# Kernel optimization log

Measured on AMD Instinct MI355X. Metric: run time of the kernel, lower is better.

The kernel has to match this reference:

```python
import jax, jax.numpy as jnp
import numpy as np

B, T, I, H = 4, 512, 128, 128


def _lstm(x, Wih, Whh, b):
    """Standard LSTM (PyTorch gate order i,f,g,o). x: [B,T,I] -> h: [B,T,H]."""
    xg = jnp.swapaxes(x, 0, 1) @ Wih.T + b  # [T,B,4H] input projections precomputed
    Hh = Whh.shape[1]
    h0 = jnp.zeros((x.shape[0], Hh), x.dtype)
    c0 = jnp.zeros((x.shape[0], Hh), x.dtype)

    def step(carry, xg_t):
        h, c = carry
        g = xg_t + h @ Whh.T
        i, f, gg, o = jnp.split(g, 4, axis=-1)
        c = jax.nn.sigmoid(f) * c + jax.nn.sigmoid(i) * jnp.tanh(gg)
        h = jax.nn.sigmoid(o) * jnp.tanh(c)
        return (h, c), h

    _, hs = jax.lax.scan(step, (h0, c0), xg)
    return jnp.swapaxes(hs, 0, 1)  # [B,T,H]


def setup_inputs() -> dict:
    key = jax.random.key(0)
    ks = jax.random.split(key, 12)
    s = 0.1
    return {
        "x": jax.random.normal(ks[0], (B, T, I), jnp.float32),
        # shared LSTM
        "Wih_s": jax.random.normal(ks[1], (4 * H, I), jnp.float32) * s,
        "Whh_s": jax.random.normal(ks[2], (4 * H, H), jnp.float32) * s,
        "b_lstm_s": jnp.zeros((4 * H,), jnp.float32),
        # Ws split along its concatenated input [x_sub; h_t; h_sub]
        "Wx": jax.random.normal(ks[3], (I, H), jnp.float32) * s,
        "Wht": jax.random.normal(ks[4], (H, H), jnp.float32) * s,
        "Whs": jax.random.normal(ks[5], (H, H), jnp.float32) * s,
        "bs": jnp.zeros((H,), jnp.float32),
        # Us: H -> 1
        "u": jax.random.normal(ks[6], (H,), jnp.float32) * s,
        "bu": jnp.zeros((), jnp.float32),
        # task LSTM over [x; R] (input_size + hidden_size)
        "Wih_t": jax.random.normal(ks[7], (4 * H, I + H), jnp.float32) * s,
        "Whh_t": jax.random.normal(ks[8], (4 * H, H), jnp.float32) * s,
        "b_lstm_t": jnp.zeros((4 * H,), jnp.float32),
    }


def reference(x, Wih_s, Whh_s, b_lstm_s, Wx, Wht, Whs, bs, u, bu,
              Wih_t, Whh_t, b_lstm_t):
    # 1) shared LSTM encoding
    Hsh = _lstm(x, Wih_s, Whh_s, b_lstm_s)  # [B,T,H]

    # 2) pairwise attention scores S[b,t,s] = Us(tanh(Ws([x_s; h_t; h_s])))
    #    decompose Ws over its concatenated input to avoid building the concat
    xp = x @ Wx          # [B,T,H] (indexed by s)
    hp_t = Hsh @ Wht     # [B,T,H] (indexed by t)
    hp_s = Hsh @ Whs     # [B,T,H] (indexed by s)
    # M[b,t,s,:]: [B,T,T,H] — the dominant (memory-bound) intermediate
    M = jnp.tanh(hp_t[:, :, None, :] + (xp + hp_s)[:, None, :, :] + bs)
    scores = jnp.einsum("btsh,h->bts", M, u) + bu  # [B,T,T]

    # 3) softmax over sub_t and weighted sum of shared outputs
    beta = jax.nn.softmax(scores, axis=-1)         # [B,T,T]
    R = jnp.einsum("bts,bsh->bth", beta, Hsh)      # [B,T,H]

    # 4) task-specific LSTM consuming the input and the aggregated message
    h_task = _lstm(jnp.concatenate([x, R], axis=-1), Wih_t, Whh_t, b_lstm_t)
    return h_task  # [B,T,H]
```

## Files before the change

### kernel.cpp

```cpp
#include <hip/hip_runtime.h>
#include <hip/hip_bf16.h>
#include <math.h>

#define Bq 4
#define Tq 512
#define Hq 128

typedef _Float16 f16x4 __attribute__((ext_vector_type(4)));
typedef _Float16 f16x8 __attribute__((ext_vector_type(8)));
typedef float f32x4 __attribute__((ext_vector_type(4)));

__device__ __forceinline__ float rcp_fast(float x) { return __builtin_amdgcn_rcpf(x); }
__device__ __forceinline__ float sigmoid_fast(float x) {
    return rcp_fast(1.0f + __expf(-x));
}
__device__ __forceinline__ float tanh_fast(float x) {
    float e = __expf(2.0f * x);
    return 1.0f - 2.0f * rcp_fast(e + 1.0f);
}

__device__ __forceinline__ void gemm_nt_body(float (*As)[68], float (*Ws)[68],
                                             const float* __restrict__ A, int lda,
                                             const float* __restrict__ W, int ldw,
                                             const float* __restrict__ bias,
                                             float* __restrict__ C, int acc_flag,
                                             int m0, int n0, int tid) {
    int tx = tid & 15, ty = tid >> 4;
    float acc[4][4] = {};
    for (int kc = 0; kc < 2; kc++) {
        __syncthreads();
#pragma unroll
        for (int i = 0; i < 4; i++) {
            int idx = tid + 256 * i;
            int r = idx >> 4, c4 = idx & 15;
            *(float4*)(&As[r][c4 * 4]) = *(const float4*)(A + (size_t)(m0 + r) * lda + kc * 64 + c4 * 4);
            *(float4*)(&Ws[r][c4 * 4]) = *(const float4*)(W + (size_t)(n0 + r) * ldw + kc * 64 + c4 * 4);
        }
        __syncthreads();
#pragma unroll
        for (int k4 = 0; k4 < 16; k4++) {
            float4 a[4], wv[4];
#pragma unroll
            for (int i = 0; i < 4; i++) a[i] = *(const float4*)(&As[ty * 4 + i][k4 * 4]);
#pragma unroll
            for (int j = 0; j < 4; j++) wv[j] = *(const float4*)(&Ws[tx * 4 + j][k4 * 4]);
#pragma unroll
            for (int i = 0; i < 4; i++)
#pragma unroll
                for (int j = 0; j < 4; j++)
                    acc[i][j] += a[i].x * wv[j].x + a[i].y * wv[j].y + a[i].z * wv[j].z + a[i].w * wv[j].w;
        }
    }
#pragma unroll
    for (int i = 0; i < 4; i++) {
        int m = m0 + ty * 4 + i;
        int n = n0 + tx * 4;
        float4 v = make_float4(acc[i][0], acc[i][1], acc[i][2], acc[i][3]);
        if (bias) { v.x += bias[n]; v.y += bias[n + 1]; v.z += bias[n + 2]; v.w += bias[n + 3]; }
        if (acc_flag) {
            float4 o = *(const float4*)(C + (size_t)m * 512 + n);
            v.x += o.x; v.y += o.y; v.z += o.z; v.w += o.w;
        }
        *(float4*)(C + (size_t)m * 512 + n) = v;
    }
}

__device__ __forceinline__ void gemm_nt_512(float (*As)[68], float (*Ws)[68],
                                            const float* __restrict__ A, int lda,
                                            const float* __restrict__ W, int ldw,
                                            const float* __restrict__ bias,
                                            float* __restrict__ C,
                                            int m0, int n0, int tid) {
    int tx = tid & 15, ty = tid >> 4;
    float acc[2][4] = {};
    for (int kc = 0; kc < 2; kc++) {
        __syncthreads();
#pragma unroll
        for (int i = 0; i < 2; i++) {
            int idx = tid + 512 * i;
            int r = idx >> 4, c4 = idx & 15;
            *(float4*)(&As[r][c4 * 4]) = *(const float4*)(A + (size_t)(m0 + r) * lda + kc * 64 + c4 * 4);
            *(float4*)(&Ws[r][c4 * 4]) = *(const float4*)(W + (size_t)(n0 + r) * ldw + kc * 64 + c4 * 4);
        }
        __syncthreads();
#pragma unroll
        for (int k4 = 0; k4 < 16; k4++) {
            float4 a[2], wv[4];
#pragma unroll
            for (int i = 0; i < 2; i++) a[i] = *(const float4*)(&As[ty * 2 + i][k4 * 4]);
#pragma unroll
            for (int j = 0; j < 4; j++) wv[j] = *(const float4*)(&Ws[tx * 4 + j][k4 * 4]);
#pragma unroll
            for (int i = 0; i < 2; i++)
#pragma unroll
                for (int j = 0; j < 4; j++)
                    acc[i][j] += a[i].x * wv[j].x + a[i].y * wv[j].y + a[i].z * wv[j].z + a[i].w * wv[j].w;
        }
    }
#pragma unroll
    for (int i = 0; i < 2; i++) {
        int m = m0 + ty * 2 + i;
        int n = n0 + tx * 4;
        float4 v = make_float4(acc[i][0], acc[i][1], acc[i][2], acc[i][3]);
        if (bias) { v.x += bias[n]; v.y += bias[n + 1]; v.z += bias[n + 2]; v.w += bias[n + 3]; }
        *(float4*)(C + (size_t)m * 512 + n) = v;
    }
}

__global__ __launch_bounds__(256) void prep(const float* __restrict__ x,
                                            const float* __restrict__ Wih_s,
                                            const float* __restrict__ b_s,
                                            const float* __restrict__ Whh_s,
                                            float* __restrict__ xg_s,
                                            _Float16* __restrict__ W16_s) {
    __shared__ __align__(16) float As[64][68];
    __shared__ __align__(16) float Ws[64][68];
    int bid = blockIdx.x;
    int tid = threadIdx.x;
    if (bid < 256) {
        gemm_nt_body(As, Ws, x, 128, Wih_s, 128, b_s, xg_s, 0,
                     (bid & 31) * 64, (bid >> 5) * 64, tid);
    } else {
        int cb = bid - 256;
        int i = (cb * 256 + tid) * 4;
        float4 v = *(const float4*)(Whh_s + i);
        f16x4 o;
        o[0] = (_Float16)v.x; o[1] = (_Float16)v.y;
        o[2] = (_Float16)v.z; o[3] = (_Float16)v.w;
        *(f16x4*)(W16_s + i) = o;
    }
}

__global__ __launch_bounds__(256) void gemm_nt(const float* __restrict__ A, int lda,
                                               const float* __restrict__ W, int ldw,
                                               const float* __restrict__ bias,
                                               float* __restrict__ C, int acc_flag) {
    __shared__ __align__(16) float As[64][68];
    __shared__ __align__(16) float Ws[64][68];
    gemm_nt_body(As, Ws, A, lda, W, ldw, bias, C, acc_flag,
                 blockIdx.x * 64, blockIdx.y * 64, threadIdx.x);
}

__global__ __launch_bounds__(256) void mid(const float* __restrict__ x,
                                           const float* __restrict__ Hsh,
                                           const float* __restrict__ Wht,
                                           const float* __restrict__ Wx,
                                           const float* __restrict__ Whs,
                                           const float* __restrict__ bs,
                                           float* __restrict__ hp_t,
                                           float* __restrict__ tc_sT) {
    __shared__ __align__(16) float As[64][68];
    __shared__ __align__(16) float Bs[64][68];
    int bid = blockIdx.x;
    int cfg = bid >> 6;
    int b2 = bid & 63;
    int m0 = (b2 & 31) * 64, n0 = (b2 >> 5) * 64;
    const float* A1 = cfg ? x : Hsh;
    const float* B1 = cfg ? Wx : Wht;
    const float* A2 = cfg ? Hsh : nullptr;
    const float* B2 = cfg ? Whs : nullptr;

    int tid = threadIdx.x;
    int tx = tid & 15, ty = tid >> 4;
    float acc[4][4] = {};
    for (int src = 0; src < 2; src++) {
        const float* A = src ? A2 : A1;
        const float* Bm = src ? B2 : B1;
        if (!A) break;
        for (int kc = 0; kc < 2; kc++) {
            __syncthreads();
#pragma unroll
            for (int i = 0; i < 4; i++) {
                int idx = tid + 256 * i;
                int r = idx >> 4, c4 = idx & 15;
                *(float4*)(&As[r][c4 * 4]) = *(const float4*)(A + (size_t)(m0 + r) * 128 + kc * 64 + c4 * 4);
                *(float4*)(&Bs[r][c4 * 4]) = *(const float4*)(Bm + (size_t)(kc * 64 + r) * 128 + n0 + c4 * 4);
            }
            __syncthreads();
#pragma unroll
            for (int k4 = 0; k4 < 16; k4++) {
                float4 a[4];
#pragma unroll
                for (int i = 0; i < 4; i++) a[i] = *(const float4*)(&As[ty * 4 + i][k4 * 4]);
#pragma unroll
                for (int kk = 0; kk < 4; kk++) {
                    float4 bv = *(const float4*)(&Bs[k4 * 4 + kk][tx * 4]);
#pragma unroll
                    for (int i = 0; i < 4; i++) {
                        float av = (kk == 0) ? a[i].x : (kk == 1) ? a[i].y : (kk == 2) ? a[i].z : a[i].w;
                        acc[i][0] += av * bv.x;
                        acc[i][1] += av * bv.y;
                        acc[i][2] += av * bv.z;
                        acc[i][3] += av * bv.w;
                    }
                }
            }
        }
    }
    if (cfg == 0) {
#pragma unroll
        for (int i = 0; i < 4; i++) {
            int m = m0 + ty * 4 + i;
            int n = n0 + tx * 4;
            *(float4*)(hp_t + (size_t)m * 128 + n) =
                make_float4(acc[i][0], acc[i][1], acc[i][2], acc[i][3]);
        }
    } else {
        __syncthreads();
#pragma unroll
        for (int i = 0; i < 4; i++)
#pragma unroll
            for (int j = 0; j < 4; j++)
                As[ty * 4 + i][tx * 4 + j] = tanh_fast(acc[i][j] + bs[n0 + tx * 4 + j]);
        __syncthreads();
        int b = m0 >> 9;
        int s0 = m0 & 511;
        int lane = tid & 63, wv = tid >> 6;
#pragma unroll 4
        for (int it = 0; it < 16; ++it) {
            int nl = wv * 16 + it;
            tc_sT[((size_t)(b * 128 + n0 + nl)) * 512 + s0 + lane] = As[lane][nl];
        }
    }
}

#define MF0(ACC, A, B) \
    asm("v_mfma_f32_16x16x32_f16 %0, %1, %2, %3" : "=&v"(ACC) : "v"(A), "a"(B), "v"(zro));
#define MF(ACC, A, B) \
    asm("v_mfma_f32_16x16x32_f16 %0, %1, %2, %0" : "+v"(ACC) : "v"(A), "a"(B));

#define LSTM_STEP(X0, X1, X2, X3, R0, R1, R2, R3, WPTR, PXG)                       \
    {                                                                              \
        f16x8 a0 = *(R0); f16x8 a1 = *(R1);                                        \
        f16x8 a2 = *(R2); f16x8 a3 = *(R3);                                        \
        float o0 = X0, o1 = X1, o2 = X2, o3 = X3;                                  \
        X0 = (PXG)[0]; X1 = (PXG)[128]; X2 = (PXG)[256]; X3 = (PXG)[384];          \
        (PXG) += 1024;                                                             \
        f32x4 ac0a, ac1a, ac2a, ac3a, ac0b, ac1b, ac2b, ac3b;                      \
        MF0(ac0a, a0, b00) MF0(ac1a, a0, b10) MF0(ac2a, a0, b20) MF0(ac3a, a0, b30)\
        MF0(ac0b, a2, b02) MF0(ac1b, a2, b12) MF0(ac2b, a2, b22) MF0(ac3b, a2, b32)\
        MF(ac0a, a1, b01) MF(ac1a, a1, b11) MF(ac2a, a1, b21) MF(ac3a, a1, b31)    \
        MF(ac0b, a3, b03) MF(ac1b, a3, b13) MF(ac2b, a3, b23) MF(ac3b, a3, b33)    \
        __builtin_amdgcn_sched_barrier(0);                                         \
        asm volatile("s_nop 7\n\ts_nop 7"                                          \
                     :: "v"(ac0a), "v"(ac1a), "v"(ac2a), "v"(ac3a),                \
                        "v"(ac0b), "v"(ac1b), "v"(ac2b), "v"(ac3b));               \
        __builtin_amdgcn_sched_barrier(0);                                         \
        float gi = ac0a[0] + ac0b[0] + o0;                                         \
        float gf = ac1a[0] + ac1b[0] + o1;                                         \
        float gg = ac2a[0] + ac2b[0] + o2;                                         \
        float go = ac3a[0] + ac3b[0] + o3;                                         \
        float si = sigmoid_fast(gi), sf = sigmoid_fast(gf), so = sigmoid_fast(go); \
        float tg = tanh_fast(gg);                                                  \
        c = sf * c + si * tg;                                                      \
        float h = so * tanh_fast(c);                                               \
        *(WPTR) = (_Float16)h;                                                     \
        *pH = h; pH += Hq;                                                         \
        __builtin_amdgcn_sched_barrier(0);                                         \
        asm volatile("s_waitcnt lgkmcnt(0)");                                      \
        __builtin_amdgcn_s_barrier();                                              \
        __builtin_amdgcn_sched_barrier(0);                                         \
    }

__device__ __forceinline__ void lstm_core(const float* __restrict__ xg,
                                          const _Float16* __restrict__ W16,
                                          float* __restrict__ Hout,
                                          _Float16* hbase, int tid) {
    int w = tid >> 6, lane = tid & 63;
    int r = lane & 15, kg = lane >> 4;
    int ch = 16 * w + r;

    for (int i = tid; i < 4096; i += 512) hbase[i] = (_Float16)0.f;

    const _Float16* wb = W16 + (size_t)ch * 128 + kg * 8;
#define LWB(g, kb) *(const f16x8*)(wb + (size_t)(g) * 16384 + (kb) * 32)
    f16x8 b00 = LWB(0, 0), b01 = LWB(0, 1), b02 = LWB(0, 2), b03 = LWB(0, 3);
    f16x8 b10 = LWB(1, 0), b11 = LWB(1, 1), b12 = LWB(1, 2), b13 = LWB(1, 3);
    f16x8 b20 = LWB(2, 0), b21 = LWB(2, 1), b22 = LWB(2, 2), b23 = LWB(2, 3);
    f16x8 b30 = LWB(3, 0), b31 = LWB(3, 1), b32 = LWB(3, 2), b33 = LWB(3, 3);
#undef LWB
    f32x4 zro = {0.f, 0.f, 0.f, 0.f};
    asm volatile(""
                 : "+a"(b00), "+a"(b01), "+a"(b02), "+a"(b03),
                   "+a"(b10), "+a"(b11), "+a"(b12), "+a"(b13),
                   "+a"(b20), "+a"(b21), "+a"(b22), "+a"(b23),
                   "+a"(b30), "+a"(b31), "+a"(b32), "+a"(b33),
                   "+v"(zro));

    int aoff0 = r * 128 + (((0 * 4 + kg) ^ r) << 3);
    int aoff1 = r * 128 + (((1 * 4 + kg) ^ r) << 3);
    int aoff2 = r * 128 + (((2 * 4 + kg) ^ r) << 3);
    int aoff3 = r * 128 + (((3 * 4 + kg) ^ r) << 3);
    int woff = (4 * kg) * 128 + (((ch >> 3) ^ (4 * kg)) << 3) + (ch & 7);

    const f16x8* rA0 = (const f16x8*)(hbase + aoff0);
    const f16x8* rA1 = (const f16x8*)(hbase + aoff1);
    const f16x8* rA2 = (const f16x8*)(hbase + aoff2);
    const f16x8* rA3 = (const f16x8*)(hbase + aoff3);
    const f16x8* rB0 = (const f16x8*)(hbase + 2048 + aoff0);
    const f16x8* rB1 = (const f16x8*)(hbase + 2048 + aoff1);
    const f16x8* rB2 = (const f16x8*)(hbase + 2048 + aoff2);
    const f16x8* rB3 = (const f16x8*)(hbase + 2048 + aoff3);
    _Float16* wA = hbase + 2048 + woff;
    _Float16* wB = hbase + woff;

    size_t kgTq = (size_t)kg * Tq;
    const float* p0 = xg + (kgTq + 0) * 512 + ch;
    const float* p1 = xg + (kgTq + 1) * 512 + ch;
    float xa0 = p0[0], xa1 = p0[128], xa2 = p0[256], xa3 = p0[384];
    float xb0 = p1[0], xb1 = p1[128], xb2 = p1[256], xb3 = p1[384];
    const float* pA = xg + (kgTq + 2) * 512 + ch;
    const float* pB = xg + (kgTq + 3) * 512 + ch;
    float* pH = Hout + kgTq * Hq + ch;

    float c = 0.f;
    __syncthreads();

    for (int t = 0; t < Tq; t += 2) {
        LSTM_STEP(xa0, xa1, xa2, xa3, rA0, rA1, rA2, rA3, wA, pA)
        LSTM_STEP(xb0, xb1, xb2, xb3, rB0, rB1, rB2, rB3, wB, pB)
    }
}

__global__ __launch_bounds__(512)
__attribute__((amdgpu_waves_per_eu(2, 2)))
void lstm_fused(const float* __restrict__ xg_s,
                const _Float16* __restrict__ W16_s,
                float* __restrict__ Hsh,
                const float* __restrict__ x,
                const float* __restrict__ Wih_t,
                const float* __restrict__ b_t,
                const float* __restrict__ Whh_t,
                float* __restrict__ xg_t,
                _Float16* __restrict__ W16_t) {
    __shared__ __align__(16) float smem[2][64][68];
    int bid = blockIdx.x;
    int tid = threadIdx.x;
    if (bid == 0) {
        lstm_core(xg_s, W16_s, Hsh, (_Float16*)&smem[0][0][0], tid);
    } else if (bid <= 256) {
        int b2 = bid - 1;
        gemm_nt_512(smem[0], smem[1], x, 128, Wih_t, 256, b_t, xg_t,
                    (b2 & 31) * 64, (b2 >> 5) * 64, tid);
    } else {
        int cb = bid - 257;
        int i = (cb * 512 + tid) * 2;
        float2 v = *(const float2*)(Whh_t + i);
        W16_t[i] = (_Float16)v.x;
        W16_t[i + 1] = (_Float16)v.y;
    }
}

__global__ __launch_bounds__(512)
__attribute__((amdgpu_waves_per_eu(2, 2)))
void lstm_b4(const float* __restrict__ xg,
             const _Float16* __restrict__ W16,
             float* __restrict__ Hout) {
    __shared__ _Float16 hbuf[2][16][128];
    lstm_core(xg, W16, Hout, &hbuf[0][0][0], threadIdx.x);
}

__global__ __launch_bounds__(512) void attn_kernel(const float* __restrict__ hp_t,
                                                   const float* __restrict__ tc_sT,
                                                   const float* __restrict__ u,
                                                   const float* __restrict__ Hsh,
                                                   float* __restrict__ R) {
    int t0 = blockIdx.x * 4;
    int b = blockIdx.y;
    int tid = threadIdx.x;
    int tq = tid >> 7, th = tid & 127;

    __shared__ __align__(16) float pa_lds[4][128];
    __shared__ __align__(16) float u_lds[128];
    __shared__ __align__(16) float sc[4][512];
    __shared__ __align__(16) float red[8];

    pa_lds[tq][th] = tanh_fast(hp_t[((size_t)b * Tq + t0 + tq) * Hq + th]);
    if (tid < 128) u_lds[tid] = u[tid];
    __syncthreads();

    const float* pc = tc_sT + (size_t)b * 65536 + 4 * th;
    const float* pa = &pa_lds[tq][0];
    float acc0 = 0.f, acc1 = 0.f, acc2 = 0.f, acc3 = 0.f;
#pragma unroll 4
    for (int h = 0; h < 128; ++h) {
        float4 qv = *(const float4*)pc;
        float p = pa[h], uu = u_lds[h];
        float n0 = p + qv.x, n1 = p + qv.y, n2 = p + qv.z, n3 = p + qv.w;
        float d0 = fmaf(p, qv.x, 1.0f), d1 = fmaf(p, qv.y, 1.0f);
        float d2 = fmaf(p, qv.z, 1.0f), d3 = fmaf(p, qv.w, 1.0f);
        acc0 = fmaf(uu * n0, rcp_fast(d0), acc0);
        acc1 = fmaf(uu * n1, rcp_fast(d1), acc1);
        acc2 = fmaf(uu * n2, rcp_fast(d2), acc2);
        acc3 = fmaf(uu * n3, rcp_fast(d3), acc3);
        pc += 512;
    }
    float p0 = __expf(acc0), p1 = __expf(acc1);
    float p2 = __expf(acc2), p3 = __expf(acc3);
    *(float4*)&sc[tq][4 * th] = make_float4(p0, p1, p2, p3);

    float psum = p0 + p1 + p2 + p3;
#pragma unroll
    for (int off = 1; off < 64; off <<= 1) psum += __shfl_xor(psum, off, 64);
    int wv = tid >> 6;
    if ((tid & 63) == 0) red[wv] = psum;
    __syncthreads();
    float rinv = rcp_fast(red[2 * tq] + red[2 * tq + 1]);

    const float* hb = Hsh + (size_t)b * Tq * Hq + th;
    const float* scp = &sc[tq][0];
    float acc = 0.0f;
#pragma unroll 4
    for (int s = 0; s < 512; ++s) {
        acc = fmaf(scp[s], hb[(size_t)s * Hq], acc);
    }
    R[((size_t)b * Tq + t0 + tq) * Hq + th] = acc * rinv;
}

extern "C" void kernel_launch(void* const* d_in, const int* in_sizes, int n_in,
                              void* d_out, int out_size, void* d_ws, size_t ws_size,
                              hipStream_t stream) {
    const float* x      = (const float*)d_in[0];
    const float* Wih_s  = (const float*)d_in[1];
    const float* Whh_s  = (const float*)d_in[2];
    const float* b_s    = (const float*)d_in[3];
    const float* Wx     = (const float*)d_in[4];
    const float* Wht    = (const float*)d_in[5];
    const float* Whs    = (const float*)d_in[6];
    const float* bs     = (const float*)d_in[7];
    const float* u      = (const float*)d_in[8];
    const float* Wih_t  = (const float*)d_in[10];
    const float* Whh_t  = (const float*)d_in[11];
    const float* b_t    = (const float*)d_in[12];
    float* out = (float*)d_out;

    float* ws    = (float*)d_ws;
    float* xg_s  = ws;
    float* xg_t  = ws + 1048576;
    float* Hsh   = ws + 2097152;
    float* hp_t  = ws + 2359296;
    float* tc_sT = ws + 2621440;
    float* Rbuf  = ws + 2883584;
    _Float16* W16_t = (_Float16*)(ws + 3145728);
    _Float16* W16_s = (_Float16*)hp_t;

    dim3 blk(256);

    prep<<<320, blk, 0, stream>>>(x, Wih_s, b_s, Whh_s, xg_s, W16_s);

    lstm_fused<<<321, 512, 0, stream>>>(xg_s, W16_s, Hsh,
                                        x, Wih_t, b_t, Whh_t, xg_t, W16_t);

    mid<<<128, blk, 0, stream>>>(x, Hsh, Wht, Wx, Whs, bs, hp_t, tc_sT);

    attn_kernel<<<dim3(Tq / 4, Bq), 512, 0, stream>>>(hp_t, tc_sT, u, Hsh, Rbuf);

    gemm_nt<<<dim3(32, 8), blk, 0, stream>>>(Rbuf, 128, Wih_t + 128, 256, nullptr, xg_t, 1);

    lstm_b4<<<1, 512, 0, stream>>>(xg_t, W16_t, out);
}
```

Measured before the change: 576.6 us.

## Split LSTM gates across two wave groups with LDS exchange, 1024-thread blocks

The sequential LSTM recurrence now runs with 1024 threads instead of 512. Each half of the waves computes two of the four gate matmuls, so a wave issues 8 MFMAs per step instead of 16. One group sends tanh(g) and sigmoid(o) through LDS to the group that updates c and h. This costs an extra barrier per timestep, and the GEMM and conversion helpers are reshaped to fit the larger block.

Measured after the change: 680.5 us. 1.18x slower.

```diff
diff --git a/kernel.cpp b/kernel.cpp
--- a/kernel.cpp
+++ b/kernel.cpp
@@ -65,46 +65,37 @@
     }
 }
 
-__device__ __forceinline__ void gemm_nt_512(float (*As)[68], float (*Ws)[68],
-                                            const float* __restrict__ A, int lda,
-                                            const float* __restrict__ W, int ldw,
-                                            const float* __restrict__ bias,
-                                            float* __restrict__ C,
-                                            int m0, int n0, int tid) {
+__device__ __forceinline__ void gemm_nt_1024(float (*As)[68], float (*Ws)[68],
+                                             const float* __restrict__ A, int lda,
+                                             const float* __restrict__ W, int ldw,
+                                             const float* __restrict__ bias,
+                                             float* __restrict__ C,
+                                             int m0, int n0, int tid) {
     int tx = tid & 15, ty = tid >> 4;
-    float acc[2][4] = {};
+    float acc[4] = {};
     for (int kc = 0; kc < 2; kc++) {
         __syncthreads();
-#pragma unroll
-        for (int i = 0; i < 2; i++) {
-            int idx = tid + 512 * i;
-            int r = idx >> 4, c4 = idx & 15;
+        {
+            int r = tid >> 4, c4 = tid & 15;
             *(float4*)(&As[r][c4 * 4]) = *(const float4*)(A + (size_t)(m0 + r) * lda + kc * 64 + c4 * 4);
             *(float4*)(&Ws[r][c4 * 4]) = *(const float4*)(W + (size_t)(n0 + r) * ldw + kc * 64 + c4 * 4);
         }
         __syncthreads();
 #pragma unroll
         for (int k4 = 0; k4 < 16; k4++) {
-            float4 a[2], wv[4];
-#pragma unroll
-            for (int i = 0; i < 2; i++) a[i] = *(const float4*)(&As[ty * 2 + i][k4 * 4]);
-#pragma unroll
-            for (int j = 0; j < 4; j++) wv[j] = *(const float4*)(&Ws[tx * 4 + j][k4 * 4]);
-#pragma unroll
-            for (int i = 0; i < 2; i++)
-#pragma unroll
-                for (int j = 0; j < 4; j++)
-                    acc[i][j] += a[i].x * wv[j].x + a[i].y * wv[j].y + a[i].z * wv[j].z + a[i].w * wv[j].w;
-        }
-    }
-#pragma unroll
-    for (int i = 0; i < 2; i++) {
-        int m = m0 + ty * 2 + i;
-        int n = n0 + tx * 4;
-        float4 v = make_float4(acc[i][0], acc[i][1], acc[i][2], acc[i][3]);
-        if (bias) { v.x += bias[n]; v.y += bias[n + 1]; v.z += bias[n + 2]; v.w += bias[n + 3]; }
-        *(float4*)(C + (size_t)m * 512 + n) = v;
-    }
+            float4 a = *(const float4*)(&As[ty][k4 * 4]);
+#pragma unroll
+            for (int j = 0; j < 4; j++) {
+                float4 wv = *(const float4*)(&Ws[tx * 4 + j][k4 * 4]);
+                acc[j] += a.x * wv.x + a.y * wv.y + a.z * wv.z + a.w * wv.w;
+            }
+        }
+    }
+    int m = m0 + ty;
+    int n = n0 + tx * 4;
+    float4 v = make_float4(acc[0], acc[1], acc[2], acc[3]);
+    if (bias) { v.x += bias[n]; v.y += bias[n + 1]; v.z += bias[n + 2]; v.w += bias[n + 3]; }
+    *(float4*)(C + (size_t)m * 512 + n) = v;
 }
 
 __global__ __launch_bounds__(256) void prep(const float* __restrict__ x,
@@ -229,33 +220,44 @@
 #define MF(ACC, A, B) \
     asm("v_mfma_f32_16x16x32_f16 %0, %1, %2, %0" : "+v"(ACC) : "v"(A), "a"(B));
 
-#define LSTM_STEP(X0, X1, X2, X3, R0, R1, R2, R3, WPTR, PXG)                       \
+#define LSTM_STEP(X0, X1, R0, R1, R2, R3, WPTR, PXG)                               \
     {                                                                              \
         f16x8 a0 = *(R0); f16x8 a1 = *(R1);                                        \
         f16x8 a2 = *(R2); f16x8 a3 = *(R3);                                        \
-        float o0 = X0, o1 = X1, o2 = X2, o3 = X3;                                  \
-        X0 = (PXG)[0]; X1 = (PXG)[128]; X2 = (PXG)[256]; X3 = (PXG)[384];          \
+        float o0 = X0, o1 = X1;                                                    \
+        X0 = (PXG)[0]; X1 = (PXG)[128];                                            \
         (PXG) += 1024;                                                             \
-        f32x4 ac0a, ac1a, ac2a, ac3a, ac0b, ac1b, ac2b, ac3b;                      \
-        MF0(ac0a, a0, b00) MF0(ac1a, a0, b10) MF0(ac2a, a0, b20) MF0(ac3a, a0, b30)\
-        MF0(ac0b, a2, b02) MF0(ac1b, a2, b12) MF0(ac2b, a2, b22) MF0(ac3b, a2, b32)\
-        MF(ac0a, a1, b01) MF(ac1a, a1, b11) MF(ac2a, a1, b21) MF(ac3a, a1, b31)    \
-        MF(ac0b, a3, b03) MF(ac1b, a3, b13) MF(ac2b, a3, b23) MF(ac3b, a3, b33)    \
+        f32x4 ac0a, ac0b, ac1a, ac1b;                                              \
+        MF0(ac0a, a0, bg00) MF0(ac1a, a0, bg10)                                    \
+        MF0(ac0b, a2, bg02) MF0(ac1b, a2, bg12)                                    \
+        MF(ac0a, a1, bg01) MF(ac1a, a1, bg11)                                      \
+        MF(ac0b, a3, bg03) MF(ac1b, a3, bg13)                                      \
         __builtin_amdgcn_sched_barrier(0);                                         \
         asm volatile("s_nop 7\n\ts_nop 7"                                          \
-                     :: "v"(ac0a), "v"(ac1a), "v"(ac2a), "v"(ac3a),                \
-                        "v"(ac0b), "v"(ac1b), "v"(ac2b), "v"(ac3b));               \
-        __builtin_amdgcn_sched_barrier(0);                                         \
-        float gi = ac0a[0] + ac0b[0] + o0;                                         \
-        float gf = ac1a[0] + ac1b[0] + o1;                                         \
-        float gg = ac2a[0] + ac2b[0] + o2;                                         \
-        float go = ac3a[0] + ac3b[0] + o3;                                         \
-        float si = sigmoid_fast(gi), sf = sigmoid_fast(gf), so = sigmoid_fast(go); \
-        float tg = tanh_fast(gg);                                                  \
-        c = sf * c + si * tg;                                                      \
-        float h = so * tanh_fast(c);                                               \
-        *(WPTR) = (_Float16)h;                                                     \
-        *pH = h; pH += Hq;                                                         \
+                     :: "v"(ac0a), "v"(ac0b), "v"(ac1a), "v"(ac1b));               \
+        __builtin_amdgcn_sched_barrier(0);                                         \
+        float g0 = ac0a[0] + ac0b[0] + o0;                                         \
+        float g1 = ac1a[0] + ac1b[0] + o1;                                         \
+        float si = 0.f, sf = 0.f;                                                  \
+        if (gp) {                                                                  \
+            float tg = tanh_fast(g0);                                              \
+            float so = sigmoid_fast(g1);                                           \
+            exch[exidx] = make_float2(tg, so);                                     \
+        } else {                                                                   \
+            si = sigmoid_fast(g0);                                                 \
+            sf = sigmoid_fast(g1);                                                 \
+        }                                                                          \
+        __builtin_amdgcn_sched_barrier(0);                                         \
+        asm volatile("s_waitcnt lgkmcnt(0)");                                      \
+        __builtin_amdgcn_s_barrier();                                              \
+        __builtin_amdgcn_sched_barrier(0);                                         \
+        if (!gp) {                                                                 \
+            float2 e = exch[exidx];                                                \
+            c = sf * c + si * e.x;                                                 \
+            float h = e.y * tanh_fast(c);                                          \
+            *(WPTR) = (_Float16)h;                                                 \
+            *pH = h; pH += Hq;                                                     \
+        }                                                                          \
         __builtin_amdgcn_sched_barrier(0);                                         \
         asm volatile("s_waitcnt lgkmcnt(0)");                                      \
         __builtin_amdgcn_s_barrier();                                              \
@@ -265,26 +267,24 @@
 __device__ __forceinline__ void lstm_core(const float* __restrict__ xg,
                                           const _Float16* __restrict__ W16,
                                           float* __restrict__ Hout,
-                                          _Float16* hbase, int tid) {
-    int w = tid >> 6, lane = tid & 63;
+                                          _Float16* hbase, float2* exch, int tid) {
+    int wid = tid >> 6, lane = tid & 63;
+    int w8 = wid & 7, gp = wid >> 3;
     int r = lane & 15, kg = lane >> 4;
-    int ch = 16 * w + r;
-
-    for (int i = tid; i < 4096; i += 512) hbase[i] = (_Float16)0.f;
-
-    const _Float16* wb = W16 + (size_t)ch * 128 + kg * 8;
+    int ch = 16 * w8 + r;
+    int exidx = w8 * 64 + lane;
+
+    for (int i = tid; i < 4096; i += 1024) hbase[i] = (_Float16)0.f;
+
+    const _Float16* wb = W16 + (size_t)((2 * gp) * 128 + ch) * 128 + kg * 8;
 #define LWB(g, kb) *(const f16x8*)(wb + (size_t)(g) * 16384 + (kb) * 32)
-    f16x8 b00 = LWB(0, 0), b01 = LWB(0, 1), b02 = LWB(0, 2), b03 = LWB(0, 3);
-    f16x8 b10 = LWB(1, 0), b11 = LWB(1, 1), b12 = LWB(1, 2), b13 = LWB(1, 3);
-    f16x8 b20 = LWB(2, 0), b21 = LWB(2, 1), b22 = LWB(2, 2), b23 = LWB(2, 3);
-    f16x8 b30 = LWB(3, 0), b31 = LWB(3, 1), b32 = LWB(3, 2), b33 = LWB(3, 3);
+    f16x8 bg00 = LWB(0, 0), bg01 = LWB(0, 1), bg02 = LWB(0, 2), bg03 = LWB(0, 3);
+    f16x8 bg10 = LWB(1, 0), bg11 = LWB(1, 1), bg12 = LWB(1, 2), bg13 = LWB(1, 3);
 #undef LWB
     f32x4 zro = {0.f, 0.f, 0.f, 0.f};
     asm volatile(""
-                 : "+a"(b00), "+a"(b01), "+a"(b02), "+a"(b03),
-                   "+a"(b10), "+a"(b11), "+a"(b12), "+a"(b13),
-                   "+a"(b20), "+a"(b21), "+a"(b22), "+a"(b23),
-                   "+a"(b30), "+a"(b31), "+a"(b32), "+a"(b33),
+                 : "+a"(bg00), "+a"(bg01), "+a"(bg02), "+a"(bg03),
+                   "+a"(bg10), "+a"(bg11), "+a"(bg12), "+a"(bg13),
                    "+v"(zro));
 
     int aoff0 = r * 128 + (((0 * 4 + kg) ^ r) << 3);
@@ -305,25 +305,24 @@
     _Float16* wB = hbase + woff;
 
     size_t kgTq = (size_t)kg * Tq;
-    const float* p0 = xg + (kgTq + 0) * 512 + ch;
-    const float* p1 = xg + (kgTq + 1) * 512 + ch;
-    float xa0 = p0[0], xa1 = p0[128], xa2 = p0[256], xa3 = p0[384];
-    float xb0 = p1[0], xb1 = p1[128], xb2 = p1[256], xb3 = p1[384];
-    const float* pA = xg + (kgTq + 2) * 512 + ch;
-    const float* pB = xg + (kgTq + 3) * 512 + ch;
+    const float* p0 = xg + (kgTq + 0) * 512 + gp * 256 + ch;
+    const float* p1 = xg + (kgTq + 1) * 512 + gp * 256 + ch;
+    float xa0 = p0[0], xa1 = p0[128];
+    float xb0 = p1[0], xb1 = p1[128];
+    const float* pA = xg + (kgTq + 2) * 512 + gp * 256 + ch;
+    const float* pB = xg + (kgTq + 3) * 512 + gp * 256 + ch;
     float* pH = Hout + kgTq * Hq + ch;
 
     float c = 0.f;
     __syncthreads();
 
     for (int t = 0; t < Tq; t += 2) {
-        LSTM_STEP(xa0, xa1, xa2, xa3, rA0, rA1, rA2, rA3, wA, pA)
-        LSTM_STEP(xb0, xb1, xb2, xb3, rB0, rB1, rB2, rB3, wB, pB)
-    }
-}
-
-__global__ __launch_bounds__(512)
-__attribute__((amdgpu_waves_per_eu(2, 2)))
+        LSTM_STEP(xa0, xa1, rA0, rA1, rA2, rA3, wA, pA)
+        LSTM_STEP(xb0, xb1, rB0, rB1, rB2, rB3, wB, pB)
+    }
+}
+
+__global__ __launch_bounds__(1024)
 void lstm_fused(const float* __restrict__ xg_s,
                 const _Float16* __restrict__ W16_s,
                 float* __restrict__ Hsh,
@@ -337,27 +336,26 @@
     int bid = blockIdx.x;
     int tid = threadIdx.x;
     if (bid == 0) {
-        lstm_core(xg_s, W16_s, Hsh, (_Float16*)&smem[0][0][0], tid);
+        lstm_core(xg_s, W16_s, Hsh, (_Float16*)&smem[0][0][0],
+                  (float2*)((char*)&smem[0][0][0] + 8192), tid);
     } else if (bid <= 256) {
         int b2 = bid - 1;
-        gemm_nt_512(smem[0], smem[1], x, 128, Wih_t, 256, b_t, xg_t,
-                    (b2 & 31) * 64, (b2 >> 5) * 64, tid);
+        gemm_nt_1024(smem[0], smem[1], x, 128, Wih_t, 256, b_t, xg_t,
+                     (b2 & 31) * 64, (b2 >> 5) * 64, tid);
     } else {
         int cb = bid - 257;
-        int i = (cb * 512 + tid) * 2;
-        float2 v = *(const float2*)(Whh_t + i);
-        W16_t[i] = (_Float16)v.x;
-        W16_t[i + 1] = (_Float16)v.y;
-    }
-}
-
-__global__ __launch_bounds__(512)
-__attribute__((amdgpu_waves_per_eu(2, 2)))
+        int i = cb * 1024 + tid;
+        W16_t[i] = (_Float16)Whh_t[i];
+    }
+}
+
+__global__ __launch_bounds__(1024)
 void lstm_b4(const float* __restrict__ xg,
              const _Float16* __restrict__ W16,
              float* __restrict__ Hout) {
-    __shared__ _Float16 hbuf[2][16][128];
-    lstm_core(xg, W16, Hout, &hbuf[0][0][0], threadIdx.x);
+    __shared__ __align__(16) _Float16 hbuf[4096];
+    __shared__ __align__(16) float2 exch[512];
+    lstm_core(xg, W16, Hout, hbuf, exch, threadIdx.x);
 }
 
 __global__ __launch_bounds__(512) void attn_kernel(const float* __restrict__ hp_t,
@@ -448,8 +446,8 @@
 
     prep<<<320, blk, 0, stream>>>(x, Wih_s, b_s, Whh_s, xg_s, W16_s);
 
-    lstm_fused<<<321, 512, 0, stream>>>(xg_s, W16_s, Hsh,
-                                        x, Wih_t, b_t, Whh_t, xg_t, W16_t);
+    lstm_fused<<<321, 1024, 0, stream>>>(xg_s, W16_s, Hsh,
+                                         x, Wih_t, b_t, Whh_t, xg_t, W16_t);
 
     mid<<<128, blk, 0, stream>>>(x, Hsh, Wht, Wx, Whs, bs, hp_t, tc_sT);
 
@@ -457,5 +455,5 @@
 
     gemm_nt<<<dim3(32, 8), blk, 0, stream>>>(Rbuf, 128, Wih_t + 128, 256, nullptr, xg_t, 1);
 
-    lstm_b4<<<1, 512, 0, stream>>>(xg_t, W16_t, out);
-}
+    lstm_b4<<<1, 1024, 0, stream>>>(xg_t, W16_t, out);
+}
```
